# Performance work log

Hardware: AMD Instinct MI355X
Metric: run time of the kernel (lower is better)

## Reference

```python
import jax, jax.numpy as jnp
import numpy as np

NUM_HEADS = 16
D_MODEL = 1024
D_K = D_MODEL // NUM_HEADS
B, S = 2, 2048


def setup_inputs() -> dict:
    key = jax.random.key(0)
    ks = jax.random.split(key, 10)
    q = jax.random.normal(ks[0], (B, S, D_MODEL), dtype=jnp.float32)
    k = jax.random.normal(ks[1], (B, S, D_MODEL), dtype=jnp.float32)
    v = jax.random.normal(ks[2], (B, S, D_MODEL), dtype=jnp.float32)
    # causal mask, 1 = keep, 0 = masked (masked_fill(mask==0, -1e9))
    mask = jnp.tril(jnp.ones((S, S), dtype=jnp.int32))[None, None, :, :]
    # Linear weights ~ N(0, 0.02); biases left at torch default-ish small uniform
    std = 0.02
    Wq = jax.random.normal(ks[3], (D_MODEL, D_MODEL), dtype=jnp.float32) * std
    Wk = jax.random.normal(ks[4], (D_MODEL, D_MODEL), dtype=jnp.float32) * std
    Wv = jax.random.normal(ks[5], (D_MODEL, D_MODEL), dtype=jnp.float32) * std
    bound = 1.0 / np.sqrt(D_MODEL)
    bq = jax.random.uniform(ks[6], (D_MODEL,), jnp.float32, -bound, bound)
    bk = jax.random.uniform(ks[7], (D_MODEL,), jnp.float32, -bound, bound)
    bv = jax.random.uniform(ks[8], (D_MODEL,), jnp.float32, -bound, bound)
    return {"q": q, "k": k, "v": v, "mask": mask,
            "Wq": Wq, "bq": bq, "Wk": Wk, "bk": bk, "Wv": Wv, "bv": bv}


def reference(q, k, v, mask, Wq, bq, Wk, bk, Wv, bv):
    # projections (torch Linear: x @ W.T + b), split heads -> [B, H, S, Dk]
    def proj(x, W, b):
        y = x @ W.T + b
        return y.reshape(B, S, NUM_HEADS, D_K).transpose(0, 2, 1, 3)

    qh, kh, vh = proj(q, Wq, bq), proj(k, Wk, bk), proj(v, Wv, bv)
    scores = jnp.einsum('bhqd,bhkd->bhqk', qh, kh) / jnp.sqrt(jnp.float32(D_K))
    scores = jnp.where(mask == 0, jnp.float32(-1e9), scores)
    p = jax.nn.softmax(scores, axis=-1)
    # dropout is identity in eval mode
    x = jnp.einsum('bhqk,bhkd->bhqd', p, vh)  # [B, H, S, Dk]
    return x.transpose(0, 2, 1, 3).reshape(B, S, D_MODEL)
```

## Files before the change

kernel.cpp:

```cpp
#include <hip/hip_runtime.h>

#define B_ 2
#define H_ 16
#define S_ 2048
#define DM 1024
#define DK 64
#define NX (4096 * 1024)
#define NW (1024 * 1024)

typedef unsigned short u16;
typedef __attribute__((ext_vector_type(8))) short bf16x8;
typedef __attribute__((ext_vector_type(8))) unsigned short u16x8;
typedef __attribute__((ext_vector_type(4))) unsigned short u16x4;
typedef __attribute__((ext_vector_type(2))) unsigned int u32x2;
typedef __attribute__((ext_vector_type(4))) float f32x4;

__device__ inline u16 f2bf(float f) {
  union { float f; unsigned int u; } c; c.f = f;
  unsigned int u = c.u;
  u += 0x7fffu + ((u >> 16) & 1u);
  return (u16)(u >> 16);
}

__device__ inline u16x8 cvt8(const float* __restrict__ src) {
  const float4 a = *reinterpret_cast<const float4*>(src);
  const float4 b = *reinterpret_cast<const float4*>(src + 4);
  u16x8 r;
  r[0] = f2bf(a.x); r[1] = f2bf(a.y); r[2] = f2bf(a.z); r[3] = f2bf(a.w);
  r[4] = f2bf(b.x); r[5] = f2bf(b.y); r[6] = f2bf(b.z); r[7] = f2bf(b.w);
  return r;
}

__device__ inline void glds16(const u16* g, u16* l) {
  __builtin_amdgcn_global_load_lds(
      (const __attribute__((address_space(1))) unsigned int*)g,
      (__attribute__((address_space(3))) unsigned int*)l, 16, 0, 0);
}

__device__ inline unsigned cvtpk(float lo, float hi) {
  unsigned r;
  asm("v_cvt_pk_bf16_f32 %0, %1, %2" : "=v"(r) : "v"(lo), "v"(hi));
  return r;
}

__global__ __launch_bounds__(256) void cvt_kernel(
    const float* __restrict__ q, const float* __restrict__ k, const float* __restrict__ v,
    const float* __restrict__ Wq, const float* __restrict__ Wk, const float* __restrict__ Wv,
    u16* __restrict__ Xq, u16* __restrict__ Xk, u16* __restrict__ Xv,
    u16* __restrict__ Wqb, u16* __restrict__ Wkb, u16* __restrict__ Wvb)
{
  const int t = blockIdx.y;
  const float* src = (t == 0) ? q : (t == 1) ? k : (t == 2) ? v
                   : (t == 3) ? Wq : (t == 4) ? Wk : Wv;
  u16* dst = (t == 0) ? Xq : (t == 1) ? Xk : (t == 2) ? Xv
           : (t == 3) ? Wqb : (t == 4) ? Wkb : Wvb;
  const int n = (t < 3) ? NX : NW;
  const int idx = (blockIdx.x * 256 + threadIdx.x) * 8;
  if (idx >= n) return;
  *reinterpret_cast<u16x8*>(&dst[idx]) = cvt8(&src[idx]);
}

__global__ __launch_bounds__(256) void proj_kernel(
    const u16* __restrict__ Xq, const u16* __restrict__ Xk, const u16* __restrict__ Xv,
    const u16* __restrict__ Wqb, const u16* __restrict__ Wkb, const u16* __restrict__ Wvb,
    const float* __restrict__ bq, const float* __restrict__ bk, const float* __restrict__ bv,
    u16* __restrict__ Qh, u16* __restrict__ Kh, u16* __restrict__ Vh)
{
  const int z = blockIdx.z;
  const u16* X      = (z == 0) ? Xq : (z == 1) ? Xk : Xv;
  const u16* W      = (z == 0) ? Wqb : (z == 1) ? Wkb : Wvb;
  const float* bias = (z == 0) ? bq : (z == 1) ? bk : bv;
  u16* out          = (z == 0) ? Qh : (z == 1) ? Kh : Vh;
  const float scale = (z == 0) ? 0.18033688f : 1.0f;

  __shared__ __align__(16) u16 Xs[128 * 32];
  __shared__ __align__(16) u16 Ws[128 * 32];

  const int tid = threadIdx.x;
  const int lane = tid & 63;
  const int w = tid >> 6;
  const int wy = w >> 1, wx = w & 1;
  const int m0 = blockIdx.y * 128;
  const int n0 = blockIdx.x * 128;
  const int ml = lane & 15;
  const int qd = lane >> 4;

  f32x4 acc[4][4] = {};

  for (int kb = 0; kb < DM; kb += 32) {
    __syncthreads();
    #pragma unroll
    for (int p = 0; p < 2; ++p) {
      const int c = p * 4 + w;
      const int row = c * 16 + (lane >> 2);
      const int col = kb + (lane & 3) * 8;
      glds16(&X[(size_t)(m0 + row) * DM + col], &Xs[c * 512]);
      glds16(&W[(size_t)(n0 + row) * DM + col], &Ws[c * 512]);
    }
    __syncthreads();
    bf16x8 a[4], bfr[4];
    #pragma unroll
    for (int i = 0; i < 4; ++i)
      a[i] = *reinterpret_cast<const bf16x8*>(&Xs[(wy * 64 + i * 16 + ml) * 32 + qd * 8]);
    #pragma unroll
    for (int j = 0; j < 4; ++j)
      bfr[j] = *reinterpret_cast<const bf16x8*>(&Ws[(wx * 64 + j * 16 + ml) * 32 + qd * 8]);
    #pragma unroll
    for (int i = 0; i < 4; ++i)
      #pragma unroll
      for (int j = 0; j < 4; ++j)
        acc[i][j] = __builtin_amdgcn_mfma_f32_16x16x32_bf16(a[i], bfr[j], acc[i][j], 0, 0, 0);
  }

  #pragma unroll
  for (int j = 0; j < 4; ++j) {
    const int n = n0 + wx * 64 + j * 16 + ml;
    const float badd = bias[n];
    const int h = n >> 6, d = n & 63;
    #pragma unroll
    for (int i = 0; i < 4; ++i) {
      #pragma unroll
      for (int r = 0; r < 4; ++r) {
        const int m = m0 + wy * 64 + i * 16 + qd * 4 + r;
        const int bi = m >> 11, s = m & 2047;
        out[((bi * H_ + h) * S_ + s) * DK + d] = f2bf((acc[i][j][r] + badd) * scale);
      }
    }
  }
}

__global__ __launch_bounds__(256) void transpose_kernel(
    const u16* __restrict__ Vh, u16* __restrict__ Vt)
{
  __shared__ __align__(16) u16 T[64 * 72];
  const int t = threadIdx.x;
  const int st = blockIdx.x, bh = blockIdx.y;
  {
    const int r = t >> 2, c = (t & 3) * 16;
    const u16* src = &Vh[((size_t)bh * S_ + st * 64 + r) * DK + c];
    *reinterpret_cast<u16x8*>(&T[r * 72 + c])     = *reinterpret_cast<const u16x8*>(src);
    *reinterpret_cast<u16x8*>(&T[r * 72 + c + 8]) = *reinterpret_cast<const u16x8*>(src + 8);
  }
  __syncthreads();
  {
    const int d = t >> 2, s0 = (t & 3) * 16;
    u16x8 a, b;
    #pragma unroll
    for (int i = 0; i < 8; ++i) a[i] = T[(s0 + i) * 72 + d];
    #pragma unroll
    for (int i = 0; i < 8; ++i) b[i] = T[(s0 + 8 + i) * 72 + d];
    u16* dst = &Vt[((size_t)bh * DK + d) * S_ + st * 64 + s0];
    *reinterpret_cast<u16x8*>(dst)     = a;
    *reinterpret_cast<u16x8*>(dst + 8) = b;
  }
}

__global__ __launch_bounds__(256) void attn_kernel(
    const u16* __restrict__ Qh, const u16* __restrict__ Kh,
    const u16* __restrict__ Vt, float* __restrict__ out)
{
  __shared__ __align__(16) u16 Ks[2][64 * 64];
  __shared__ __align__(16) u16 Vs[2][64 * 64];
  __shared__ __align__(16) u16 Ps[4][2][16 * 64];

  const int tid  = threadIdx.x;
  const int lane = tid & 63;
  const int w    = tid >> 6;

  const int fid = blockIdx.x;
  const int bh  = (fid & 7) * 4 + ((fid >> 3) & 3);
  const int qt  = 15 - (fid >> 5);
  const int b   = bh >> 4, h = bh & 15;
  const int ml  = lane & 15, qd = lane >> 4;
  const int m7  = ml & 7;
  const int u0  = qd ^ m7;
  const int qh  = qd >> 1, ql = qd & 1;
  const int R0  = qt * 128;
  const int nt  = 2 * qt + 2;

  bf16x8 qa[2][2];
  #pragma unroll
  for (int g = 0; g < 2; ++g)
    #pragma unroll
    for (int ch = 0; ch < 2; ++ch)
      qa[g][ch] = *reinterpret_cast<const bf16x8*>(
          &Qh[((size_t)bh * S_ + R0 + w * 32 + g * 16 + ml) * DK + ch * 32 + qd * 8]);
  asm volatile("s_waitcnt vmcnt(0)" ::: "memory");

  const u16* kb0 = Kh + (size_t)bh * S_ * DK;
  const u16* vb0 = Vt + (size_t)bh * DK * S_;
  const int r0 = tid >> 3, r1 = r0 + 32;
  const int cs = (tid & 7) ^ (r0 & 7);
  const u16* sK0 = kb0 + r0 * DK + cs * 8;
  const u16* sK1 = kb0 + r1 * DK + cs * 8;
  const u16* sV0 = vb0 + (size_t)r0 * S_ + cs * 8;
  const u16* sV1 = vb0 + (size_t)r1 * S_ + cs * 8;

  f32x4 oacc[2][4] = {};
  float lsum[2] = {0.f, 0.f};

  glds16(sK0, &Ks[0][tid * 8]);
  glds16(sK1, &Ks[0][2048 + tid * 8]);
  glds16(sV0, &Vs[0][tid * 8]);
  glds16(sV1, &Vs[0][2048 + tid * 8]);
  sK0 += 4096; sK1 += 4096; sV0 += 64; sV1 += 64;

  int cur = 0;
  for (int t = 0; t < nt; ++t) {
    if (t + 1 < nt) {
      glds16(sK0, &Ks[cur ^ 1][tid * 8]);
      glds16(sK1, &Ks[cur ^ 1][2048 + tid * 8]);
      glds16(sV0, &Vs[cur ^ 1][tid * 8]);
      glds16(sV1, &Vs[cur ^ 1][2048 + tid * 8]);
      sK0 += 4096; sK1 += 4096; sV0 += 64; sV1 += 64;
      asm volatile("s_waitcnt vmcnt(4)" ::: "memory");
    } else {
      asm volatile("s_waitcnt vmcnt(0)" ::: "memory");
    }
    __builtin_amdgcn_s_barrier();
    asm volatile("" ::: "memory");

    const u16* Kb = Ks[cur];
    const u16* Vb = Vs[cur];

    const int d16_0 = (R0 + w * 32 - t * 64) >> 4;
    const int d16_1 = d16_0 + 1;
    const int jtop  = (d16_1 < 3) ? d16_1 : 3;

    if (jtop >= 0) {
      #pragma unroll
      for (int j = 0; j < 4; ++j) {
        if (j > jtop) break;
        const int rk = (j * 16 + ml) * 64;
        const bf16x8 k0 = *reinterpret_cast<const bf16x8*>(&Kb[rk + u0 * 8]);
        const bf16x8 k1 = *reinterpret_cast<const bf16x8*>(&Kb[rk + (u0 ^ 4) * 8]);
        #pragma unroll
        for (int g = 0; g < 2; ++g) {
          const int d16g = d16_0 + g;
          if (j > d16g) continue;
          f32x4 zz = {};
          zz = __builtin_amdgcn_mfma_f32_16x16x32_bf16(k0, qa[g][0], zz, 0, 0, 0);
          zz = __builtin_amdgcn_mfma_f32_16x16x32_bf16(k1, qa[g][1], zz, 0, 0, 0);
          if (j == d16g) {
            #pragma unroll
            for (int r = 0; r < 4; ++r)
              if (qd * 4 + r > ml) zz[r] = -1e30f;
          }
          const float e0 = __builtin_amdgcn_exp2f(zz[0]);
          const float e1 = __builtin_amdgcn_exp2f(zz[1]);
          const float e2 = __builtin_amdgcn_exp2f(zz[2]);
          const float e3 = __builtin_amdgcn_exp2f(zz[3]);
          lsum[g] += (e0 + e1) + (e2 + e3);
          u32x2 pk;
          pk[0] = cvtpk(e0, e1);
          pk[1] = cvtpk(e2, e3);
          *reinterpret_cast<u32x2*>(
              &Ps[w][g][ml * 64 + (((2 * j + qh) ^ m7) * 8) + ql * 4]) = pk;
        }
      }
      #pragma unroll
      for (int g = 0; g < 2; ++g) {
        const int d16g = d16_0 + g;
        if (d16g == 0 || d16g == 2) {
          const int jz = d16g + 1;
          *reinterpret_cast<u32x2*>(
              &Ps[w][g][ml * 64 + (((2 * jz + qh) ^ m7) * 8) + ql * 4]) = (u32x2){0, 0};
        }
      }
      #pragma unroll
      for (int c = 0; c < 2; ++c) {
        const bool use0 = d16_0 >= 2 * c;
        const bool use1 = d16_1 >= 2 * c;
        if (!(use0 | use1)) continue;
        bf16x8 vb[4];
        #pragma unroll
        for (int dj = 0; dj < 4; ++dj)
          vb[dj] = *reinterpret_cast<const bf16x8*>(
              &Vb[(dj * 16 + ml) * 64 + (u0 ^ (c << 2)) * 8]);
        if (use0) {
          const bf16x8 pa = *reinterpret_cast<const bf16x8*>(
              &Ps[w][0][ml * 64 + (u0 ^ (c << 2)) * 8]);
          #pragma unroll
          for (int dj = 0; dj < 4; ++dj)
            oacc[0][dj] = __builtin_amdgcn_mfma_f32_16x16x32_bf16(pa, vb[dj], oacc[0][dj], 0, 0, 0);
        }
        if (use1) {
          const bf16x8 pa = *reinterpret_cast<const bf16x8*>(
              &Ps[w][1][ml * 64 + (u0 ^ (c << 2)) * 8]);
          #pragma unroll
          for (int dj = 0; dj < 4; ++dj)
            oacc[1][dj] = __builtin_amdgcn_mfma_f32_16x16x32_bf16(pa, vb[dj], oacc[1][dj], 0, 0, 0);
        }
      }
    }

    asm volatile("" ::: "memory");
    __builtin_amdgcn_s_barrier();
    asm volatile("" ::: "memory");
    cur ^= 1;
  }

  #pragma unroll
  for (int g = 0; g < 2; ++g) {
    float lg = lsum[g];
    lg += __shfl_xor(lg, 16, 64);
    lg += __shfl_xor(lg, 32, 64);
    #pragma unroll
    for (int r = 0; r < 4; ++r) {
      const float inv = 1.0f / __shfl(lg, qd * 4 + r, 64);
      const int srow = R0 + w * 32 + g * 16 + qd * 4 + r;
      float* op = &out[(size_t)(b * S_ + srow) * DM + h * DK + ml];
      #pragma unroll
      for (int dj = 0; dj < 4; ++dj)
        op[dj * 16] = oacc[g][dj][r] * inv;
    }
  }
}

extern "C" void kernel_launch(void* const* d_in, const int* in_sizes, int n_in,
                              void* d_out, int out_size, void* d_ws, size_t ws_size,
                              hipStream_t stream) {
  const float* q  = (const float*)d_in[0];
  const float* k  = (const float*)d_in[1];
  const float* v  = (const float*)d_in[2];
  const float* Wq = (const float*)d_in[4];
  const float* bq = (const float*)d_in[5];
  const float* Wk = (const float*)d_in[6];
  const float* bk = (const float*)d_in[7];
  const float* Wv = (const float*)d_in[8];
  const float* bv = (const float*)d_in[9];

  u16* Xq  = (u16*)d_ws;
  u16* Xk  = Xq + NX;
  u16* Xv  = Xk + NX;
  u16* Wqb = Xv + NX;
  u16* Wkb = Wqb + NW;
  u16* Wvb = Wkb + NW;
  u16* Qh  = Wvb + NW;
  u16* Kh  = Qh + NX;
  u16* Vh  = Kh + NX;
  u16* Vt  = Xq;

  cvt_kernel<<<dim3(NX / (256 * 8), 6), 256, 0, stream>>>(
      q, k, v, Wq, Wk, Wv, Xq, Xk, Xv, Wqb, Wkb, Wvb);
  proj_kernel<<<dim3(DM / 128, (B_ * S_) / 128, 3), 256, 0, stream>>>(
      Xq, Xk, Xv, Wqb, Wkb, Wvb, bq, bk, bv, Qh, Kh, Vh);
  transpose_kernel<<<dim3(S_ / 64, B_ * H_), 256, 0, stream>>>(Vh, Vt);
  attn_kernel<<<dim3(512), 256, 0, stream>>>(
      Qh, Kh, Vt, (float*)d_out);
}
```

Baseline: 215.7 us.

## Fuse V transpose into projection epilogue and load V fragments directly from global

The V projection epilogue now writes its output directly in transposed [B,H,Dk,S] layout using packed 4-element stores, so the separate transpose kernel and its launch go away. The attention kernel drops the shared-memory staging of V and loads V fragments straight from global into registers each iteration. The QK MFMAs are split from the softmax so all score tiles are computed first. s_setprio is raised around the MFMA blocks. The trade-offs are uncached, non-LDS V loads sitting on the critical path, adjusted vmcnt waits that must match the load counts, and higher register pressure.

```diff
diff --git a/kernel.cpp b/kernel.cpp
--- a/kernel.cpp
+++ b/kernel.cpp
@@ -64,13 +64,13 @@
     const u16* __restrict__ Xq, const u16* __restrict__ Xk, const u16* __restrict__ Xv,
     const u16* __restrict__ Wqb, const u16* __restrict__ Wkb, const u16* __restrict__ Wvb,
     const float* __restrict__ bq, const float* __restrict__ bk, const float* __restrict__ bv,
-    u16* __restrict__ Qh, u16* __restrict__ Kh, u16* __restrict__ Vh)
+    u16* __restrict__ Qh, u16* __restrict__ Kh, u16* __restrict__ Vt)
 {
   const int z = blockIdx.z;
   const u16* X      = (z == 0) ? Xq : (z == 1) ? Xk : Xv;
   const u16* W      = (z == 0) ? Wqb : (z == 1) ? Wkb : Wvb;
   const float* bias = (z == 0) ? bq : (z == 1) ? bk : bv;
-  u16* out          = (z == 0) ? Qh : (z == 1) ? Kh : Vh;
+  u16* out          = (z == 0) ? Qh : (z == 1) ? Kh : Vt;
   const float scale = (z == 0) ? 0.18033688f : 1.0f;
 
   __shared__ __align__(16) u16 Xs[128 * 32];
@@ -112,46 +112,38 @@
         acc[i][j] = __builtin_amdgcn_mfma_f32_16x16x32_bf16(a[i], bfr[j], acc[i][j], 0, 0, 0);
   }
 
-  #pragma unroll
-  for (int j = 0; j < 4; ++j) {
-    const int n = n0 + wx * 64 + j * 16 + ml;
-    const float badd = bias[n];
-    const int h = n >> 6, d = n & 63;
-    #pragma unroll
-    for (int i = 0; i < 4; ++i) {
-      #pragma unroll
-      for (int r = 0; r < 4; ++r) {
-        const int m = m0 + wy * 64 + i * 16 + qd * 4 + r;
-        const int bi = m >> 11, s = m & 2047;
-        out[((bi * H_ + h) * S_ + s) * DK + d] = f2bf((acc[i][j][r] + badd) * scale);
-      }
-    }
-  }
-}
-
-__global__ __launch_bounds__(256) void transpose_kernel(
-    const u16* __restrict__ Vh, u16* __restrict__ Vt)
-{
-  __shared__ __align__(16) u16 T[64 * 72];
-  const int t = threadIdx.x;
-  const int st = blockIdx.x, bh = blockIdx.y;
-  {
-    const int r = t >> 2, c = (t & 3) * 16;
-    const u16* src = &Vh[((size_t)bh * S_ + st * 64 + r) * DK + c];
-    *reinterpret_cast<u16x8*>(&T[r * 72 + c])     = *reinterpret_cast<const u16x8*>(src);
-    *reinterpret_cast<u16x8*>(&T[r * 72 + c + 8]) = *reinterpret_cast<const u16x8*>(src + 8);
-  }
-  __syncthreads();
-  {
-    const int d = t >> 2, s0 = (t & 3) * 16;
-    u16x8 a, b;
-    #pragma unroll
-    for (int i = 0; i < 8; ++i) a[i] = T[(s0 + i) * 72 + d];
-    #pragma unroll
-    for (int i = 0; i < 8; ++i) b[i] = T[(s0 + 8 + i) * 72 + d];
-    u16* dst = &Vt[((size_t)bh * DK + d) * S_ + st * 64 + s0];
-    *reinterpret_cast<u16x8*>(dst)     = a;
-    *reinterpret_cast<u16x8*>(dst + 8) = b;
+  if (z == 2) {
+    #pragma unroll
+    for (int j = 0; j < 4; ++j) {
+      const int n = n0 + wx * 64 + j * 16 + ml;
+      const float badd = bias[n];
+      const int h = n >> 6, d = n & 63;
+      #pragma unroll
+      for (int i = 0; i < 4; ++i) {
+        const int mb = m0 + wy * 64 + i * 16 + qd * 4;
+        const int bi = mb >> 11, s0 = mb & 2047;
+        u16x4 pk;
+        #pragma unroll
+        for (int r = 0; r < 4; ++r) pk[r] = f2bf(acc[i][j][r] + badd);
+        *reinterpret_cast<u16x4*>(&out[((size_t)(bi * H_ + h) * DK + d) * S_ + s0]) = pk;
+      }
+    }
+  } else {
+    #pragma unroll
+    for (int j = 0; j < 4; ++j) {
+      const int n = n0 + wx * 64 + j * 16 + ml;
+      const float badd = bias[n];
+      const int h = n >> 6, d = n & 63;
+      #pragma unroll
+      for (int i = 0; i < 4; ++i) {
+        #pragma unroll
+        for (int r = 0; r < 4; ++r) {
+          const int m = m0 + wy * 64 + i * 16 + qd * 4 + r;
+          const int bi = m >> 11, s = m & 2047;
+          out[((bi * H_ + h) * S_ + s) * DK + d] = f2bf((acc[i][j][r] + badd) * scale);
+        }
+      }
+    }
   }
 }
 
@@ -160,7 +152,6 @@
     const u16* __restrict__ Vt, float* __restrict__ out)
 {
   __shared__ __align__(16) u16 Ks[2][64 * 64];
-  __shared__ __align__(16) u16 Vs[2][64 * 64];
   __shared__ __align__(16) u16 Ps[4][2][16 * 64];
 
   const int tid  = threadIdx.x;
@@ -188,59 +179,83 @@
   asm volatile("s_waitcnt vmcnt(0)" ::: "memory");
 
   const u16* kb0 = Kh + (size_t)bh * S_ * DK;
-  const u16* vb0 = Vt + (size_t)bh * DK * S_;
+  const u16* vbase = Vt + (size_t)bh * DK * S_;
   const int r0 = tid >> 3, r1 = r0 + 32;
   const int cs = (tid & 7) ^ (r0 & 7);
   const u16* sK0 = kb0 + r0 * DK + cs * 8;
   const u16* sK1 = kb0 + r1 * DK + cs * 8;
-  const u16* sV0 = vb0 + (size_t)r0 * S_ + cs * 8;
-  const u16* sV1 = vb0 + (size_t)r1 * S_ + cs * 8;
 
   f32x4 oacc[2][4] = {};
   float lsum[2] = {0.f, 0.f};
 
   glds16(sK0, &Ks[0][tid * 8]);
   glds16(sK1, &Ks[0][2048 + tid * 8]);
-  glds16(sV0, &Vs[0][tid * 8]);
-  glds16(sV1, &Vs[0][2048 + tid * 8]);
-  sK0 += 4096; sK1 += 4096; sV0 += 64; sV1 += 64;
+  sK0 += 4096; sK1 += 4096;
+
+  const u16* vrow = vbase + (size_t)ml * S_ + qd * 8;
 
   int cur = 0;
   for (int t = 0; t < nt; ++t) {
+    bf16x8 vf[2][4];
+    #pragma unroll
+    for (int c = 0; c < 2; ++c)
+      #pragma unroll
+      for (int dj = 0; dj < 4; ++dj)
+        vf[c][dj] = *reinterpret_cast<const bf16x8*>(
+            vrow + (size_t)(dj * 16) * S_ + t * 64 + c * 32);
+
     if (t + 1 < nt) {
       glds16(sK0, &Ks[cur ^ 1][tid * 8]);
       glds16(sK1, &Ks[cur ^ 1][2048 + tid * 8]);
-      glds16(sV0, &Vs[cur ^ 1][tid * 8]);
-      glds16(sV1, &Vs[cur ^ 1][2048 + tid * 8]);
-      sK0 += 4096; sK1 += 4096; sV0 += 64; sV1 += 64;
-      asm volatile("s_waitcnt vmcnt(4)" ::: "memory");
+      sK0 += 4096; sK1 += 4096;
+      asm volatile("s_waitcnt vmcnt(10)" ::: "memory");
     } else {
-      asm volatile("s_waitcnt vmcnt(0)" ::: "memory");
+      asm volatile("s_waitcnt vmcnt(8)" ::: "memory");
     }
     __builtin_amdgcn_s_barrier();
     asm volatile("" ::: "memory");
 
     const u16* Kb = Ks[cur];
-    const u16* Vb = Vs[cur];
 
     const int d16_0 = (R0 + w * 32 - t * 64) >> 4;
     const int d16_1 = d16_0 + 1;
     const int jtop  = (d16_1 < 3) ? d16_1 : 3;
 
     if (jtop >= 0) {
+      bf16x8 kf[4][2];
       #pragma unroll
       for (int j = 0; j < 4; ++j) {
         if (j > jtop) break;
         const int rk = (j * 16 + ml) * 64;
-        const bf16x8 k0 = *reinterpret_cast<const bf16x8*>(&Kb[rk + u0 * 8]);
-        const bf16x8 k1 = *reinterpret_cast<const bf16x8*>(&Kb[rk + (u0 ^ 4) * 8]);
+        kf[j][0] = *reinterpret_cast<const bf16x8*>(&Kb[rk + u0 * 8]);
+        kf[j][1] = *reinterpret_cast<const bf16x8*>(&Kb[rk + (u0 ^ 4) * 8]);
+      }
+
+      f32x4 sfr[2][4];
+      __builtin_amdgcn_s_setprio(1);
+      #pragma unroll
+      for (int j = 0; j < 4; ++j) {
+        if (j > jtop) break;
         #pragma unroll
         for (int g = 0; g < 2; ++g) {
           const int d16g = d16_0 + g;
           if (j > d16g) continue;
           f32x4 zz = {};
-          zz = __builtin_amdgcn_mfma_f32_16x16x32_bf16(k0, qa[g][0], zz, 0, 0, 0);
-          zz = __builtin_amdgcn_mfma_f32_16x16x32_bf16(k1, qa[g][1], zz, 0, 0, 0);
+          zz = __builtin_amdgcn_mfma_f32_16x16x32_bf16(kf[j][0], qa[g][0], zz, 0, 0, 0);
+          zz = __builtin_amdgcn_mfma_f32_16x16x32_bf16(kf[j][1], qa[g][1], zz, 0, 0, 0);
+          sfr[g][j] = zz;
+        }
+      }
+      __builtin_amdgcn_s_setprio(0);
+
+      #pragma unroll
+      for (int j = 0; j < 4; ++j) {
+        if (j > jtop) break;
+        #pragma unroll
+        for (int g = 0; g < 2; ++g) {
+          const int d16g = d16_0 + g;
+          if (j > d16g) continue;
+          f32x4 zz = sfr[g][j];
           if (j == d16g) {
             #pragma unroll
             for (int r = 0; r < 4; ++r)
@@ -267,30 +282,28 @@
               &Ps[w][g][ml * 64 + (((2 * jz + qh) ^ m7) * 8) + ql * 4]) = (u32x2){0, 0};
         }
       }
+
       #pragma unroll
       for (int c = 0; c < 2; ++c) {
         const bool use0 = d16_0 >= 2 * c;
         const bool use1 = d16_1 >= 2 * c;
         if (!(use0 | use1)) continue;
-        bf16x8 vb[4];
-        #pragma unroll
-        for (int dj = 0; dj < 4; ++dj)
-          vb[dj] = *reinterpret_cast<const bf16x8*>(
-              &Vb[(dj * 16 + ml) * 64 + (u0 ^ (c << 2)) * 8]);
+        __builtin_amdgcn_s_setprio(1);
         if (use0) {
           const bf16x8 pa = *reinterpret_cast<const bf16x8*>(
               &Ps[w][0][ml * 64 + (u0 ^ (c << 2)) * 8]);
           #pragma unroll
           for (int dj = 0; dj < 4; ++dj)
-            oacc[0][dj] = __builtin_amdgcn_mfma_f32_16x16x32_bf16(pa, vb[dj], oacc[0][dj], 0, 0, 0);
+            oacc[0][dj] = __builtin_amdgcn_mfma_f32_16x16x32_bf16(pa, vf[c][dj], oacc[0][dj], 0, 0, 0);
         }
         if (use1) {
           const bf16x8 pa = *reinterpret_cast<const bf16x8*>(
               &Ps[w][1][ml * 64 + (u0 ^ (c << 2)) * 8]);
           #pragma unroll
           for (int dj = 0; dj < 4; ++dj)
-            oacc[1][dj] = __builtin_amdgcn_mfma_f32_16x16x32_bf16(pa, vb[dj], oacc[1][dj], 0, 0, 0);
-        }
+            oacc[1][dj] = __builtin_amdgcn_mfma_f32_16x16x32_bf16(pa, vf[c][dj], oacc[1][dj], 0, 0, 0);
+        }
+        __builtin_amdgcn_s_setprio(0);
       }
     }
 
@@ -338,14 +351,12 @@
   u16* Wvb = Wkb + NW;
   u16* Qh  = Wvb + NW;
   u16* Kh  = Qh + NX;
-  u16* Vh  = Kh + NX;
-  u16* Vt  = Xq;
+  u16* Vt  = Kh + NX;
 
   cvt_kernel<<<dim3(NX / (256 * 8), 6), 256, 0, stream>>>(
       q, k, v, Wq, Wk, Wv, Xq, Xk, Xv, Wqb, Wkb, Wvb);
   proj_kernel<<<dim3(DM / 128, (B_ * S_) / 128, 3), 256, 0, stream>>>(
-      Xq, Xk, Xv, Wqb, Wkb, Wvb, bq, bk, bv, Qh, Kh, Vh);
-  transpose_kernel<<<dim3(S_ / 64, B_ * H_), 256, 0, stream>>>(Vh, Vt);
+      Xq, Xk, Xv, Wqb, Wkb, Wvb, bq, bk, bv, Qh, Kh, Vt);
   attn_kernel<<<dim3(512), 256, 0, stream>>>(
       Qh, Kh, Vt, (float*)d_out);
 }
```

Result: slower. 247.5 us (+14.7%).

## Switch attention to 32x32 MFMA with register-resident P via permlane swap

Applied to the files above, without the earlier changes.

Rewrites the attention inner loop to use 32x32x16 bf16 MFMAs for both QK^T and PV. The probability tile now stays in registers and is rearranged with permlane32_swap instead of a round trip through shared memory. It also reorders the query-tile schedule to interleave long and short causal tiles, and adds s_setprio around the MFMA blocks. The aim is to remove LDS traffic and instruction overhead for P and to balance work across blocks. The cost is higher register pressure from the 16-wide accumulators, plus a small LDS buffer for the final normalisation.

```diff
diff --git a/kernel.cpp b/kernel.cpp
--- a/kernel.cpp
+++ b/kernel.cpp
@@ -13,7 +13,9 @@
 typedef __attribute__((ext_vector_type(8))) unsigned short u16x8;
 typedef __attribute__((ext_vector_type(4))) unsigned short u16x4;
 typedef __attribute__((ext_vector_type(2))) unsigned int u32x2;
+typedef __attribute__((ext_vector_type(4))) unsigned int u32x4;
 typedef __attribute__((ext_vector_type(4))) float f32x4;
+typedef __attribute__((ext_vector_type(16))) float f32x16;
 
 __device__ inline u16 f2bf(float f) {
   union { float f; unsigned int u; } c; c.f = f;
@@ -42,6 +44,22 @@
   asm("v_cvt_pk_bf16_f32 %0, %1, %2" : "=v"(r) : "v"(lo), "v"(hi));
   return r;
 }
+
+#if __has_builtin(__builtin_amdgcn_permlane32_swap)
+__device__ inline void plswap(unsigned& a, unsigned& b) {
+  auto r = __builtin_amdgcn_permlane32_swap(a, b, false, false);
+  a = r[0]; b = r[1];
+}
+#else
+__device__ inline void plswap(unsigned& a, unsigned& b) {
+  const unsigned pa = (unsigned)__shfl_xor((int)a, 32, 64);
+  const unsigned pb = (unsigned)__shfl_xor((int)b, 32, 64);
+  const bool hi = (threadIdx.x & 32) != 0;
+  const unsigned na = hi ? pb : a;
+  const unsigned nb = hi ? b : pa;
+  a = na; b = nb;
+}
+#endif
 
 __global__ __launch_bounds__(256) void cvt_kernel(
     const float* __restrict__ q, const float* __restrict__ k, const float* __restrict__ v,
@@ -161,30 +179,29 @@
 {
   __shared__ __align__(16) u16 Ks[2][64 * 64];
   __shared__ __align__(16) u16 Vs[2][64 * 64];
-  __shared__ __align__(16) u16 Ps[4][2][16 * 64];
+  __shared__ float Ls[4][32];
 
   const int tid  = threadIdx.x;
   const int lane = tid & 63;
   const int w    = tid >> 6;
+  const int l31  = lane & 31, hi = lane >> 5;
+  const int x7   = l31 & 7;
 
   const int fid = blockIdx.x;
   const int bh  = (fid & 7) * 4 + ((fid >> 3) & 3);
-  const int qt  = 15 - (fid >> 5);
+  const int qtl = fid >> 5;
+  const int qt  = (qtl < 8) ? (15 - 2 * qtl) : (2 * (qtl - 8));
   const int b   = bh >> 4, h = bh & 15;
-  const int ml  = lane & 15, qd = lane >> 4;
-  const int m7  = ml & 7;
-  const int u0  = qd ^ m7;
-  const int qh  = qd >> 1, ql = qd & 1;
   const int R0  = qt * 128;
   const int nt  = 2 * qt + 2;
 
-  bf16x8 qa[2][2];
-  #pragma unroll
-  for (int g = 0; g < 2; ++g)
-    #pragma unroll
-    for (int ch = 0; ch < 2; ++ch)
-      qa[g][ch] = *reinterpret_cast<const bf16x8*>(
-          &Qh[((size_t)bh * S_ + R0 + w * 32 + g * 16 + ml) * DK + ch * 32 + qd * 8]);
+  bf16x8 qa[4];
+  {
+    const u16* qp = &Qh[((size_t)bh * S_ + R0 + w * 32 + l31) * DK + hi * 8];
+    #pragma unroll
+    for (int s = 0; s < 4; ++s)
+      qa[s] = *reinterpret_cast<const bf16x8*>(qp + s * 16);
+  }
   asm volatile("s_waitcnt vmcnt(0)" ::: "memory");
 
   const u16* kb0 = Kh + (size_t)bh * S_ * DK;
@@ -196,8 +213,8 @@
   const u16* sV0 = vb0 + (size_t)r0 * S_ + cs * 8;
   const u16* sV1 = vb0 + (size_t)r1 * S_ + cs * 8;
 
-  f32x4 oacc[2][4] = {};
-  float lsum[2] = {0.f, 0.f};
+  f32x16 oacc0 = {}, oacc1 = {};
+  float lsum = 0.f;
 
   glds16(sK0, &Ks[0][tid * 8]);
   glds16(sK1, &Ks[0][2048 + tid * 8]);
@@ -223,74 +240,70 @@
     const u16* Kb = Ks[cur];
     const u16* Vb = Vs[cur];
 
-    const int d16_0 = (R0 + w * 32 - t * 64) >> 4;
-    const int d16_1 = d16_0 + 1;
-    const int jtop  = (d16_1 < 3) ? d16_1 : 3;
-
-    if (jtop >= 0) {
-      #pragma unroll
-      for (int j = 0; j < 4; ++j) {
-        if (j > jtop) break;
-        const int rk = (j * 16 + ml) * 64;
-        const bf16x8 k0 = *reinterpret_cast<const bf16x8*>(&Kb[rk + u0 * 8]);
-        const bf16x8 k1 = *reinterpret_cast<const bf16x8*>(&Kb[rk + (u0 ^ 4) * 8]);
+    const int base  = R0 + w * 32 - t * 64;
+    const int ksmax = (base + 31) >> 5;
+    const int ksm   = (ksmax > 1) ? 1 : ksmax;
+
+    if (ksm >= 0) {
+      f32x16 sfr[2];
+      __builtin_amdgcn_s_setprio(1);
+      #pragma unroll
+      for (int ks = 0; ks < 2; ++ks) {
+        if (ks > ksm) break;
+        const int rb = (ks * 32 + l31) * 64;
+        f32x16 sf = {};
         #pragma unroll
-        for (int g = 0; g < 2; ++g) {
-          const int d16g = d16_0 + g;
-          if (j > d16g) continue;
-          f32x4 zz = {};
-          zz = __builtin_amdgcn_mfma_f32_16x16x32_bf16(k0, qa[g][0], zz, 0, 0, 0);
-          zz = __builtin_amdgcn_mfma_f32_16x16x32_bf16(k1, qa[g][1], zz, 0, 0, 0);
-          if (j == d16g) {
-            #pragma unroll
-            for (int r = 0; r < 4; ++r)
-              if (qd * 4 + r > ml) zz[r] = -1e30f;
-          }
-          const float e0 = __builtin_amdgcn_exp2f(zz[0]);
-          const float e1 = __builtin_amdgcn_exp2f(zz[1]);
-          const float e2 = __builtin_amdgcn_exp2f(zz[2]);
-          const float e3 = __builtin_amdgcn_exp2f(zz[3]);
-          lsum[g] += (e0 + e1) + (e2 + e3);
-          u32x2 pk;
-          pk[0] = cvtpk(e0, e1);
-          pk[1] = cvtpk(e2, e3);
-          *reinterpret_cast<u32x2*>(
-              &Ps[w][g][ml * 64 + (((2 * j + qh) ^ m7) * 8) + ql * 4]) = pk;
+        for (int s = 0; s < 4; ++s) {
+          const bf16x8 af = *reinterpret_cast<const bf16x8*>(
+              &Kb[rb + ((2 * s + hi) ^ x7) * 8]);
+          sf = __builtin_amdgcn_mfma_f32_32x32x16_bf16(af, qa[s], sf, 0, 0, 0);
+        }
+        sfr[ks] = sf;
+      }
+      __builtin_amdgcn_s_setprio(0);
+
+      unsigned pku[2][4][2];
+      #pragma unroll
+      for (int ks = 0; ks < 2; ++ks) {
+        if (ks > ksm) break;
+        const int Dg = base + l31 - 32 * ks - 4 * hi;
+        const bool full = (base >= 32 * ks + 31);
+        float e[16];
+        #pragma unroll
+        for (int r = 0; r < 16; ++r) {
+          const int rk = (r & 3) + 8 * (r >> 2);
+          const float ex = __builtin_amdgcn_exp2f(sfr[ks][r]);
+          e[r] = (full || rk <= Dg) ? ex : 0.f;
+        }
+        float a01 = 0.f;
+        #pragma unroll
+        for (int r = 0; r < 16; ++r) a01 += e[r];
+        lsum += a01;
+        #pragma unroll
+        for (int m = 0; m < 4; ++m) {
+          pku[ks][m][0] = cvtpk(e[4 * m], e[4 * m + 1]);
+          pku[ks][m][1] = cvtpk(e[4 * m + 2], e[4 * m + 3]);
         }
       }
-      #pragma unroll
-      for (int g = 0; g < 2; ++g) {
-        const int d16g = d16_0 + g;
-        if (d16g == 0 || d16g == 2) {
-          const int jz = d16g + 1;
-          *reinterpret_cast<u32x2*>(
-              &Ps[w][g][ml * 64 + (((2 * jz + qh) ^ m7) * 8) + ql * 4]) = (u32x2){0, 0};
-        }
-      }
-      #pragma unroll
-      for (int c = 0; c < 2; ++c) {
-        const bool use0 = d16_0 >= 2 * c;
-        const bool use1 = d16_1 >= 2 * c;
-        if (!(use0 | use1)) continue;
-        bf16x8 vb[4];
-        #pragma unroll
-        for (int dj = 0; dj < 4; ++dj)
-          vb[dj] = *reinterpret_cast<const bf16x8*>(
-              &Vb[(dj * 16 + ml) * 64 + (u0 ^ (c << 2)) * 8]);
-        if (use0) {
-          const bf16x8 pa = *reinterpret_cast<const bf16x8*>(
-              &Ps[w][0][ml * 64 + (u0 ^ (c << 2)) * 8]);
-          #pragma unroll
-          for (int dj = 0; dj < 4; ++dj)
-            oacc[0][dj] = __builtin_amdgcn_mfma_f32_16x16x32_bf16(pa, vb[dj], oacc[0][dj], 0, 0, 0);
-        }
-        if (use1) {
-          const bf16x8 pa = *reinterpret_cast<const bf16x8*>(
-              &Ps[w][1][ml * 64 + (u0 ^ (c << 2)) * 8]);
-          #pragma unroll
-          for (int dj = 0; dj < 4; ++dj)
-            oacc[1][dj] = __builtin_amdgcn_mfma_f32_16x16x32_bf16(pa, vb[dj], oacc[1][dj], 0, 0, 0);
-        }
+
+      const int smax = 2 * ksm + 1;
+      #pragma unroll
+      for (int s = 0; s < 4; ++s) {
+        if (s > smax) break;
+        const int ks = s >> 1, p = s & 1;
+        unsigned w0 = pku[ks][2 * p][0],     w1v = pku[ks][2 * p][1];
+        unsigned w2 = pku[ks][2 * p + 1][0], w3  = pku[ks][2 * p + 1][1];
+        plswap(w0, w2);
+        plswap(w1v, w3);
+        u32x4 paw; paw[0] = w0; paw[1] = w1v; paw[2] = w2; paw[3] = w3;
+        const bf16x8 pa = *reinterpret_cast<const bf16x8*>(&paw);
+        const int uv = ((2 * s + hi) ^ x7) * 8;
+        const bf16x8 vb0f = *reinterpret_cast<const bf16x8*>(&Vb[l31 * 64 + uv]);
+        const bf16x8 vb1f = *reinterpret_cast<const bf16x8*>(&Vb[(32 + l31) * 64 + uv]);
+        __builtin_amdgcn_s_setprio(1);
+        oacc0 = __builtin_amdgcn_mfma_f32_32x32x16_bf16(pa, vb0f, oacc0, 0, 0, 0);
+        oacc1 = __builtin_amdgcn_mfma_f32_32x32x16_bf16(pa, vb1f, oacc1, 0, 0, 0);
+        __builtin_amdgcn_s_setprio(0);
       }
     }
 
@@ -300,20 +313,16 @@
     cur ^= 1;
   }
 
+  const float lt = lsum + __shfl_xor(lsum, 32, 64);
+  if (hi == 0) Ls[w][l31] = 1.0f / lt;
   #pragma unroll
-  for (int g = 0; g < 2; ++g) {
-    float lg = lsum[g];
-    lg += __shfl_xor(lg, 16, 64);
-    lg += __shfl_xor(lg, 32, 64);
-    #pragma unroll
-    for (int r = 0; r < 4; ++r) {
-      const float inv = 1.0f / __shfl(lg, qd * 4 + r, 64);
-      const int srow = R0 + w * 32 + g * 16 + qd * 4 + r;
-      float* op = &out[(size_t)(b * S_ + srow) * DM + h * DK + ml];
-      #pragma unroll
-      for (int dj = 0; dj < 4; ++dj)
-        op[dj * 16] = oacc[g][dj][r] * inv;
-    }
+  for (int r = 0; r < 16; ++r) {
+    const int rq = (r & 3) + 8 * (r >> 2) + 4 * hi;
+    const float inv = Ls[w][rq];
+    const int srow = R0 + w * 32 + rq;
+    float* op = &out[(size_t)(b * S_ + srow) * DM + h * DK + l31];
+    op[0]  = oacc0[r] * inv;
+    op[32] = oacc1[r] * inv;
   }
 }
 
```

Measured after the change: 219.3 us. No clear change (+1.7%).
